# Performance work log

Hardware: AMD Instinct MI355X
Metric: run time of the kernel (lower is better)

Reference implementation:

```python
import jax, jax.numpy as jnp
import numpy as np

Q_MIN = 0.01
PT_THLD = 0.9
MAX_ETA = 4.0
LW_REP = 1.0
LW_NOISE = 0.1
LW_COWARD = 0.1
EPS = 1e-9

N_HITS = 50000
N_CLUSTERS = 1024  # cluster id 0 = noise, ids 1..K-1 = objects
D_EMB = 32


def setup_inputs() -> dict:
    key = jax.random.key(0)
    k0, k1, k2, k3, k4, k5 = jax.random.split(key, 6)
    beta = jax.random.uniform(k0, (N_HITS,), dtype=jnp.float32)
    x = jax.random.normal(k1, (N_HITS, D_EMB), dtype=jnp.float32)
    pt = jax.random.uniform(k2, (N_HITS,), dtype=jnp.float32)
    eta = jax.random.normal(k3, (N_HITS,), dtype=jnp.float32)
    reconstructable = jax.random.randint(k4, (N_HITS,), 0, 2, dtype=jnp.int32)
    cluster_ids = jax.random.randint(k5, (N_HITS,), 0, N_CLUSTERS, dtype=jnp.int64)
    return {
        'beta': beta, 'x': x, 'pt': pt, 'eta': eta,
        'reconstructable': reconstructable, 'cluster_ids': cluster_ids,
        'n_clusters': N_CLUSTERS,
    }


def reference(beta, x, pt, eta, reconstructable, cluster_ids, n_clusters):
    K = int(n_clusters)
    n_hits = beta.shape[0]
    n_part = K - 1  # objects of interest (excluding noise id 0)

    # charge q_j = arctanh(beta)^2 + q_min
    q = jnp.arctanh(jnp.clip(beta, 0.0, 1.0 - 1e-4)) ** 2 + Q_MIN  # [N]

    # attractive membership mask [N, K-1]: hit j belongs to object k and passes filters
    oids = jnp.arange(1, K)
    hit_ok = (reconstructable > 0) & (pt > PT_THLD) & (jnp.abs(eta) < MAX_ETA)
    att = (cluster_ids[:, None] == oids[None, :]) & hit_ok[:, None]
    attf = att.astype(q.dtype)

    # condensation point per object: hit with max charge within the object
    alphas = jnp.argmax(q[:, None] * attf, axis=0)  # [K-1]
    q_k = q[alphas]
    x_k = x[alphas]  # [K-1, D]

    # pairwise Euclidean distances, GEMM form (avoids [N,K,D] intermediate)
    d2 = (jnp.sum(x * x, axis=1)[:, None]
          + jnp.sum(x_k * x_k, axis=1)[None, :]
          - 2.0 * (x @ x_k.T))
    dist = jnp.sqrt(jnp.maximum(d2, 1e-12))  # [N, K-1]

    qw = q[:, None] * q_k[None, :]

    n_hits_oi = jnp.sum(hit_ok).astype(q.dtype)
    norm_att = EPS + n_hits_oi - n_part
    norm_rep = EPS + (n_part - 1) * n_hits

    v_att = jnp.sum(qw * (dist ** 2) * attf) / norm_att

    rep = (~att) & (dist < 1.0)  # max_n_rep=0 -> no subsampling
    v_rep = jnp.sum(qw * (1.0 - dist) * rep.astype(q.dtype)) / norm_rep

    l_coward = jnp.mean(1.0 - beta[alphas])

    noise_mask = (cluster_ids <= 0).astype(q.dtype)  # noise_threshold = 0
    l_noise = jnp.sum(beta * noise_mask) / jnp.maximum(jnp.sum(noise_mask), 1.0)

    total = v_att + LW_REP * v_rep + LW_NOISE * l_noise + LW_COWARD * l_coward
    return total
```

## Files before the change

kernel.cpp:

```cpp
#include <hip/hip_runtime.h>
#include <math.h>

namespace {

constexpr int D = 32;
constexpr int KOBJ = 1023;
constexpr float QMIN = 0.01f;
constexpr float PTT = 0.9f;
constexpr float METAETA = 4.0f;

typedef __attribute__((ext_vector_type(8))) short short8;
typedef __attribute__((ext_vector_type(4))) float f32x4;

__device__ inline float waveSum(float v) {
#pragma unroll
  for (int o = 32; o > 0; o >>= 1) v += __shfl_down(v, o, 64);
  return v;
}

__device__ inline ushort f2bf(float f) {
  unsigned u = __float_as_uint(f);
  return (ushort)((u + 0x7FFFu + ((u >> 16) & 1u)) >> 16);
}

__global__ void k_init(float* acc, int* flagNZ, unsigned long long* keys,
                       const int* __restrict__ cidw, int N) {
  int i = blockIdx.x * blockDim.x + threadIdx.x;
  if (i < KOBJ) keys[i] = 0ull;
  if (i < 8) acc[i] = 0.f;
  if (blockIdx.x == 0) {
    if (threadIdx.x == 0) flagNZ[0] = 0;
    __syncthreads();
    for (int jj = threadIdx.x; jj < 1024; jj += blockDim.x) {
      int idx = 2 * jj + 1;
      if (idx < N && cidw[idx] != 0) flagNZ[0] = 1;
    }
  }
}

__global__ void k_hits(const float* __restrict__ beta, const float* __restrict__ x,
                       const float* __restrict__ pt, const float* __restrict__ eta,
                       const int* __restrict__ recon, const int* __restrict__ cidw,
                       int N, const int* __restrict__ flagNZ,
                       float* acc, unsigned long long* keys,
                       float* __restrict__ qArr, float* __restrict__ nxArr,
                       int* __restrict__ attkArr) {
  int j = blockIdx.x * blockDim.x + threadIdx.x;
  int is64 = (flagNZ[0] == 0);
  bool ok = false;
  if (j < N) {
    int cid = is64 ? cidw[2 * j] : cidw[j];
    float b = beta[j];
    float bc = fminf(fmaxf(b, 0.f), 1.f - 1e-4f);
    float t = atanhf(bc);
    float q = t * t + QMIN;
    ok = (recon[j] > 0) && (pt[j] > PTT) && (fabsf(eta[j]) < METAETA);
    float nx = 0.f;
    const float4* xr = (const float4*)(x + (size_t)j * D);
#pragma unroll
    for (int i2 = 0; i2 < 8; ++i2) {
      float4 v = xr[i2];
      nx += v.x * v.x + v.y * v.y + v.z * v.z + v.w * v.w;
    }
    int attk = (ok && cid >= 1) ? cid : 0;
    qArr[j] = q;
    nxArr[j] = nx;
    attkArr[j] = attk;
    if (cid <= 0) {
      atomicAdd(&acc[2], b);
      atomicAdd(&acc[3], 1.f);
    }
    if (attk >= 1) {
      unsigned long long key =
          (((unsigned long long)__float_as_uint(q)) << 32) |
          (unsigned long long)(0xFFFFFFFFu - (unsigned)j);
      atomicMax(&keys[attk - 1], key);
    }
  }
  unsigned long long bal = __ballot(ok);
  if ((threadIdx.x & 63) == 0 && bal)
    atomicAdd(&acc[4], (float)__popcll(bal));
}

__global__ void k_clusters(const float* __restrict__ beta, const float* __restrict__ x,
                           const unsigned long long* __restrict__ keys,
                           const float* __restrict__ qArr, const float* __restrict__ nxArr,
                           int* __restrict__ alphaArr, float2* __restrict__ qnk,
                           ushort* __restrict__ xkb, float* acc) {
  int k = blockIdx.x * blockDim.x + threadIdx.x;
  float cw = 0.f;
  if (k < KOBJ) {
    unsigned long long key = keys[k];
    int alpha = (key != 0ull) ? (int)(0xFFFFFFFFu - (unsigned)(key & 0xFFFFFFFFull)) : 0;
    alphaArr[k] = alpha;
    qnk[k] = make_float2(qArr[alpha], nxArr[alpha]);
    const float4* s4 = (const float4*)(x + (size_t)alpha * D);
    ushort* dst = xkb + (size_t)k * D;
#pragma unroll
    for (int i = 0; i < 8; ++i) {
      float4 v = s4[i];
      dst[4 * i + 0] = f2bf(v.x);
      dst[4 * i + 1] = f2bf(v.y);
      dst[4 * i + 2] = f2bf(v.z);
      dst[4 * i + 3] = f2bf(v.w);
    }
    cw = 1.f - beta[alpha];
  } else if (k == KOBJ) {
    qnk[k] = make_float2(0.f, 1e30f);
    ushort* dst = xkb + (size_t)k * D;
#pragma unroll
    for (int i = 0; i < D; ++i) dst[i] = 0;
  }
  float s = waveSum(cw);
  if ((threadIdx.x & 63) == 0 && s != 0.f) atomicAdd(&acc[5], s);
}

__global__ __launch_bounds__(256) void k_pair_att(
    const float* __restrict__ x, int N, int rowgroups,
    const float* __restrict__ qArr, const float* __restrict__ nxArr,
    const int* __restrict__ attkArr, const int* __restrict__ alphaArr,
    const float2* __restrict__ qnk, const ushort* __restrict__ xkb,
    float* acc) {
  int t = threadIdx.x;

  if ((int)blockIdx.x < rowgroups) {
    __shared__ float2 qnkS[1024];
    for (int i = t; i < 1024; i += 256) qnkS[i] = qnk[i];

    int wv = t >> 6;
    int ln = t & 63;
    int lr = ln & 15;
    int lk = ln >> 4;
    int rowbase = blockIdx.x * 64;

    short8 afr[4];
#pragma unroll
    for (int rt = 0; rt < 4; ++rt) {
      int row = rowbase + rt * 16 + lr;
      row = min(row, N - 1);
      const float* p = x + (size_t)row * D + lk * 8;
      float4 v0 = *(const float4*)p;
      float4 v1 = *(const float4*)(p + 4);
      short8 a;
      a[0] = (short)f2bf(v0.x); a[1] = (short)f2bf(v0.y);
      a[2] = (short)f2bf(v0.z); a[3] = (short)f2bf(v0.w);
      a[4] = (short)f2bf(v1.x); a[5] = (short)f2bf(v1.y);
      a[6] = (short)f2bf(v1.z); a[7] = (short)f2bf(v1.w);
      afr[rt] = a;
    }
    float ha[4][4];
#pragma unroll
    for (int rt = 0; rt < 4; ++rt)
#pragma unroll
      for (int i = 0; i < 4; ++i) {
        int row = rowbase + rt * 16 + lk * 4 + i;
        ha[rt][i] = (row < N) ? (nxArr[row] - 1.f) * 0.5f : 1e37f;
      }
    __syncthreads();

    float rep = 0.f;
    int objbase = wv * 256;
#pragma unroll 1
    for (int tt = 0; tt < 16; ++tt) {
      int obj = objbase + tt * 16 + lr;
      const short8 b = *(const short8*)(xkb + (size_t)obj * D + lk * 8);
      float2 qn = qnkS[obj];
      float hk = qn.y * 0.5f;
      f32x4 z = {0.f, 0.f, 0.f, 0.f};
      f32x4 dot0 = __builtin_amdgcn_mfma_f32_16x16x32_bf16(afr[0], b, z, 0, 0, 0);
      f32x4 dot1 = __builtin_amdgcn_mfma_f32_16x16x32_bf16(afr[1], b, z, 0, 0, 0);
      f32x4 dot2 = __builtin_amdgcn_mfma_f32_16x16x32_bf16(afr[2], b, z, 0, 0, 0);
      f32x4 dot3 = __builtin_amdgcn_mfma_f32_16x16x32_bf16(afr[3], b, z, 0, 0, 0);
      float m = -1e30f;
#pragma unroll
      for (int i = 0; i < 4; ++i) {
        m = fmaxf(m, dot0[i] - (ha[0][i] + hk));
        m = fmaxf(m, dot1[i] - (ha[1][i] + hk));
        m = fmaxf(m, dot2[i] - (ha[2][i] + hk));
        m = fmaxf(m, dot3[i] - (ha[3][i] + hk));
      }
      if (__any(m > 0.f)) {
        float qk = qn.x;
        float nk1 = qn.y + 1.f;
#pragma unroll
        for (int rt = 0; rt < 4; ++rt) {
          float d0 = (rt == 0) ? dot0[0] : (rt == 1) ? dot1[0] : (rt == 2) ? dot2[0] : dot3[0];
          float d1 = (rt == 0) ? dot0[1] : (rt == 1) ? dot1[1] : (rt == 2) ? dot2[1] : dot3[1];
          float d2v = (rt == 0) ? dot0[2] : (rt == 1) ? dot1[2] : (rt == 2) ? dot2[2] : dot3[2];
          float d3 = (rt == 0) ? dot0[3] : (rt == 1) ? dot1[3] : (rt == 2) ? dot2[3] : dot3[3];
          float dd[4] = {d0, d1, d2v, d3};
#pragma unroll
          for (int i = 0; i < 4; ++i) {
            float d2 = fmaf(2.f, ha[rt][i] - dd[i], nk1);
            if (d2 < 1.f) {
              int row = rowbase + rt * 16 + lk * 4 + i;
              rep += qArr[row] * qk * (1.f - sqrtf(fmaxf(d2, 1e-12f)));
            }
          }
        }
      }
    }
    float s = waveSum(rep);
    if ((t & 63) == 0 && s != 0.f) atomicAdd(&acc[1], s);
  } else {
    int j = (blockIdx.x - rowgroups) * 256 + t;
    float attc = 0.f, repSub = 0.f;
    if (j < N) {
      int attk = attkArr[j];
      if (attk >= 1) {
        int k0 = attk - 1;
        int alpha = alphaArr[k0];
        float2 qn = qnk[k0];
        const float4* xj = (const float4*)(x + (size_t)j * D);
        const float4* xk = (const float4*)(x + (size_t)alpha * D);
        float dot = 0.f;
#pragma unroll
        for (int i = 0; i < 8; ++i) {
          float4 a = xj[i], b = xk[i];
          dot += a.x * b.x + a.y * b.y + a.z * b.z + a.w * b.w;
        }
        float d2 = nxArr[j] + qn.y - 2.f * dot;
        float w = qArr[j] * qn.x;
        attc = w * fmaxf(d2, 1e-12f);
        if (d2 < 1.f)
          repSub = w * (1.f - sqrtf(fmaxf(d2, 1e-12f)));
      }
    }
    float sa = waveSum(attc);
    float sr = waveSum(repSub);
    if ((t & 63) == 0) {
      if (sa != 0.f) atomicAdd(&acc[0], sa);
      if (sr != 0.f) atomicAdd(&acc[1], -sr);
    }
  }
}

__global__ void k_final(const float* __restrict__ acc, int N, float* out) {
  if (threadIdx.x == 0 && blockIdx.x == 0) {
    double attSum = acc[0], repSum = acc[1], noiseSum = acc[2];
    double noiseCnt = acc[3], okCnt = acc[4], cowardSum = acc[5];
    double norm_att = 1e-9 + okCnt - (double)KOBJ;
    double norm_rep = 1e-9 + (double)(KOBJ - 1) * (double)N;
    double v_att = attSum / norm_att;
    double v_rep = repSum / norm_rep;
    double l_coward = cowardSum / (double)KOBJ;
    double l_noise = noiseSum / fmax(noiseCnt, 1.0);
    out[0] = (float)(v_att + 1.0 * v_rep + 0.1 * l_noise + 0.1 * l_coward);
  }
}

}

extern "C" void kernel_launch(void* const* d_in, const int* in_sizes, int n_in,
                              void* d_out, int out_size, void* d_ws, size_t ws_size,
                              hipStream_t stream) {
  const float* beta = (const float*)d_in[0];
  const float* x = (const float*)d_in[1];
  const float* pt = (const float*)d_in[2];
  const float* eta = (const float*)d_in[3];
  const int* recon = (const int*)d_in[4];
  const int* cidw = (const int*)d_in[5];
  int N = in_sizes[0];
  float* out = (float*)d_out;

  char* w = (char*)d_ws;
  float* acc = (float*)w;
  int* flagNZ = (int*)(w + 32);
  unsigned long long* keys = (unsigned long long*)(w + 64);
  int* alphaArr = (int*)(w + 8256);
  float2* qnk = (float2*)(w + 12352);
  ushort* xkb = (ushort*)(w + 20544);
  float* qArr = (float*)(w + 86080);
  float* nxArr = (float*)(w + 86080 + (size_t)N * 4);
  int* attkArr = (int*)(w + 86080 + (size_t)N * 8);

  int nbN = (N + 255) / 256;
  int rowgroups = (N + 63) / 64;

  k_init<<<4, 256, 0, stream>>>(acc, flagNZ, keys, cidw, N);
  k_hits<<<nbN, 256, 0, stream>>>(beta, x, pt, eta, recon, cidw, N, flagNZ,
                                  acc, keys, qArr, nxArr, attkArr);
  k_clusters<<<4, 256, 0, stream>>>(beta, x, keys, qArr, nxArr,
                                    alphaArr, qnk, xkb, acc);
  k_pair_att<<<rowgroups + nbN, 256, 0, stream>>>(x, N, rowgroups, qArr, nxArr,
                                                  attkArr, alphaArr, qnk, xkb, acc);
  k_final<<<1, 64, 0, stream>>>(acc, N, out);
}
```

Baseline: 60.40 us.

## Fuse cluster and final kernels via last-block counters; fold norms into MFMA accumulator

The cluster-selection pass now runs in the last finishing block of the hits kernel, detected with a threadfence plus an atomic ticket counter. The final reduction runs the same way in the last block of the pair kernel, which removes two kernel launches. The pair kernel also merges the attractive-term blocks into the row-group blocks, with the first wave handling the 64 hits of its rows. The MFMA is seeded with nx+nk as the accumulator and x is prescaled by -2, so it outputs squared distances directly and the per-element subtract work goes away. The cost is a serialized tail in the last block, and rounding -2x to bf16 is exact, so precision is essentially unchanged.

```diff
diff --git a/kernel.cpp b/kernel.cpp
--- a/kernel.cpp
+++ b/kernel.cpp
@@ -23,11 +23,14 @@
   return (ushort)((u + 0x7FFFu + ((u >> 16) & 1u)) >> 16);
 }
 
-__global__ void k_init(float* acc, int* flagNZ, unsigned long long* keys,
-                       const int* __restrict__ cidw, int N) {
+__global__ void k_init(float* acc, unsigned* cnt, int* flagNZ,
+                       unsigned long long* keys, const int* __restrict__ cidw,
+                       int N) {
   int i = blockIdx.x * blockDim.x + threadIdx.x;
   if (i < KOBJ) keys[i] = 0ull;
   if (i < 8) acc[i] = 0.f;
+  if (i == 8) cnt[0] = 0u;
+  if (i == 9) cnt[1] = 0u;
   if (blockIdx.x == 0) {
     if (threadIdx.x == 0) flagNZ[0] = 0;
     __syncthreads();
@@ -38,22 +41,25 @@
   }
 }
 
-__global__ void k_hits(const float* __restrict__ beta, const float* __restrict__ x,
-                       const float* __restrict__ pt, const float* __restrict__ eta,
-                       const int* __restrict__ recon, const int* __restrict__ cidw,
-                       int N, const int* __restrict__ flagNZ,
-                       float* acc, unsigned long long* keys,
-                       float* __restrict__ qArr, float* __restrict__ nxArr,
-                       int* __restrict__ attkArr) {
-  int j = blockIdx.x * blockDim.x + threadIdx.x;
+__global__ __launch_bounds__(256) void k_hits_cl(
+    const float* __restrict__ beta, const float* __restrict__ x,
+    const float* __restrict__ pt, const float* __restrict__ eta,
+    const int* __restrict__ recon, const int* __restrict__ cidw,
+    int N, const int* __restrict__ flagNZ,
+    float* acc, unsigned* cnt, unsigned long long* keys,
+    float* __restrict__ qArr, float* __restrict__ nxArr,
+    int* __restrict__ attkArr, int* __restrict__ alphaArr,
+    float2* __restrict__ qnk, ushort* __restrict__ xkb) {
+  int t = threadIdx.x;
+  int j = blockIdx.x * 256 + t;
   int is64 = (flagNZ[0] == 0);
   bool ok = false;
   if (j < N) {
     int cid = is64 ? cidw[2 * j] : cidw[j];
     float b = beta[j];
     float bc = fminf(fmaxf(b, 0.f), 1.f - 1e-4f);
-    float t = atanhf(bc);
-    float q = t * t + QMIN;
+    float tt = atanhf(bc);
+    float q = tt * tt + QMIN;
     ok = (recon[j] > 0) && (pt[j] > PTT) && (fabsf(eta[j]) < METAETA);
     float nx = 0.f;
     const float4* xr = (const float4*)(x + (size_t)j * D);
@@ -78,132 +84,130 @@
     }
   }
   unsigned long long bal = __ballot(ok);
-  if ((threadIdx.x & 63) == 0 && bal)
+  if ((t & 63) == 0 && bal)
     atomicAdd(&acc[4], (float)__popcll(bal));
-}
-
-__global__ void k_clusters(const float* __restrict__ beta, const float* __restrict__ x,
-                           const unsigned long long* __restrict__ keys,
-                           const float* __restrict__ qArr, const float* __restrict__ nxArr,
-                           int* __restrict__ alphaArr, float2* __restrict__ qnk,
-                           ushort* __restrict__ xkb, float* acc) {
-  int k = blockIdx.x * blockDim.x + threadIdx.x;
+
+  __threadfence();
+  __shared__ int lastFlag;
+  if (t == 0) {
+    unsigned tk = atomicAdd(&cnt[0], 1u);
+    lastFlag = (tk == gridDim.x - 1);
+  }
+  __syncthreads();
+  if (!lastFlag) return;
+  __threadfence();
+
   float cw = 0.f;
-  if (k < KOBJ) {
-    unsigned long long key = keys[k];
-    int alpha = (key != 0ull) ? (int)(0xFFFFFFFFu - (unsigned)(key & 0xFFFFFFFFull)) : 0;
-    alphaArr[k] = alpha;
-    qnk[k] = make_float2(qArr[alpha], nxArr[alpha]);
-    const float4* s4 = (const float4*)(x + (size_t)alpha * D);
-    ushort* dst = xkb + (size_t)k * D;
-#pragma unroll
-    for (int i = 0; i < 8; ++i) {
-      float4 v = s4[i];
-      dst[4 * i + 0] = f2bf(v.x);
-      dst[4 * i + 1] = f2bf(v.y);
-      dst[4 * i + 2] = f2bf(v.z);
-      dst[4 * i + 3] = f2bf(v.w);
-    }
-    cw = 1.f - beta[alpha];
-  } else if (k == KOBJ) {
-    qnk[k] = make_float2(0.f, 1e30f);
-    ushort* dst = xkb + (size_t)k * D;
-#pragma unroll
-    for (int i = 0; i < D; ++i) dst[i] = 0;
+  for (int k = t; k < 1024; k += 256) {
+    if (k < KOBJ) {
+      unsigned long long key = keys[k];
+      int alpha = (key != 0ull) ? (int)(0xFFFFFFFFu - (unsigned)(key & 0xFFFFFFFFull)) : 0;
+      alphaArr[k] = alpha;
+      qnk[k] = make_float2(qArr[alpha], nxArr[alpha]);
+      const float4* s4 = (const float4*)(x + (size_t)alpha * D);
+      ushort* dst = xkb + (size_t)k * D;
+#pragma unroll
+      for (int i = 0; i < 8; ++i) {
+        float4 v = s4[i];
+        dst[4 * i + 0] = f2bf(v.x);
+        dst[4 * i + 1] = f2bf(v.y);
+        dst[4 * i + 2] = f2bf(v.z);
+        dst[4 * i + 3] = f2bf(v.w);
+      }
+      cw += 1.f - beta[alpha];
+    } else {
+      qnk[k] = make_float2(0.f, 1e30f);
+      ushort* dst = xkb + (size_t)k * D;
+#pragma unroll
+      for (int i = 0; i < D; ++i) dst[i] = 0;
+    }
   }
   float s = waveSum(cw);
-  if ((threadIdx.x & 63) == 0 && s != 0.f) atomicAdd(&acc[5], s);
-}
-
-__global__ __launch_bounds__(256) void k_pair_att(
-    const float* __restrict__ x, int N, int rowgroups,
+  if ((t & 63) == 0 && s != 0.f) atomicAdd(&acc[5], s);
+}
+
+__global__ __launch_bounds__(256) void k_pair_all(
+    const float* __restrict__ x, int N,
     const float* __restrict__ qArr, const float* __restrict__ nxArr,
     const int* __restrict__ attkArr, const int* __restrict__ alphaArr,
     const float2* __restrict__ qnk, const ushort* __restrict__ xkb,
-    float* acc) {
+    float* acc, unsigned* cnt, float* out) {
+  __shared__ float2 qnkS[1024];
+  __shared__ int lastFlag;
   int t = threadIdx.x;
-
-  if ((int)blockIdx.x < rowgroups) {
-    __shared__ float2 qnkS[1024];
-    for (int i = t; i < 1024; i += 256) qnkS[i] = qnk[i];
-
-    int wv = t >> 6;
-    int ln = t & 63;
-    int lr = ln & 15;
-    int lk = ln >> 4;
-    int rowbase = blockIdx.x * 64;
-
-    short8 afr[4];
-#pragma unroll
-    for (int rt = 0; rt < 4; ++rt) {
-      int row = rowbase + rt * 16 + lr;
-      row = min(row, N - 1);
-      const float* p = x + (size_t)row * D + lk * 8;
-      float4 v0 = *(const float4*)p;
-      float4 v1 = *(const float4*)(p + 4);
-      short8 a;
-      a[0] = (short)f2bf(v0.x); a[1] = (short)f2bf(v0.y);
-      a[2] = (short)f2bf(v0.z); a[3] = (short)f2bf(v0.w);
-      a[4] = (short)f2bf(v1.x); a[5] = (short)f2bf(v1.y);
-      a[6] = (short)f2bf(v1.z); a[7] = (short)f2bf(v1.w);
-      afr[rt] = a;
-    }
-    float ha[4][4];
-#pragma unroll
-    for (int rt = 0; rt < 4; ++rt)
-#pragma unroll
-      for (int i = 0; i < 4; ++i) {
-        int row = rowbase + rt * 16 + lk * 4 + i;
-        ha[rt][i] = (row < N) ? (nxArr[row] - 1.f) * 0.5f : 1e37f;
-      }
-    __syncthreads();
-
-    float rep = 0.f;
-    int objbase = wv * 256;
+  for (int i = t; i < 1024; i += 256) qnkS[i] = qnk[i];
+
+  int wv = t >> 6;
+  int ln = t & 63;
+  int lr = ln & 15;
+  int lk = ln >> 4;
+  int rowbase = blockIdx.x * 64;
+
+  short8 am2[4];
+#pragma unroll
+  for (int rt = 0; rt < 4; ++rt) {
+    int row = min(rowbase + rt * 16 + lr, N - 1);
+    const float* p = x + (size_t)row * D + lk * 8;
+    float4 v0 = *(const float4*)p;
+    float4 v1 = *(const float4*)(p + 4);
+    short8 a;
+    a[0] = (short)f2bf(-2.f * v0.x); a[1] = (short)f2bf(-2.f * v0.y);
+    a[2] = (short)f2bf(-2.f * v0.z); a[3] = (short)f2bf(-2.f * v0.w);
+    a[4] = (short)f2bf(-2.f * v1.x); a[5] = (short)f2bf(-2.f * v1.y);
+    a[6] = (short)f2bf(-2.f * v1.z); a[7] = (short)f2bf(-2.f * v1.w);
+    am2[rt] = a;
+  }
+  float nxr[4][4], qrow[4][4];
+#pragma unroll
+  for (int rt = 0; rt < 4; ++rt)
+#pragma unroll
+    for (int i = 0; i < 4; ++i) {
+      int row = rowbase + rt * 16 + lk * 4 + i;
+      int rc = min(row, N - 1);
+      nxr[rt][i] = (row < N) ? nxArr[rc] : 1e37f;
+      qrow[rt][i] = (row < N) ? qArr[rc] : 0.f;
+    }
+  __syncthreads();
+
+  float rep = 0.f;
+  int objbase = wv * 256;
 #pragma unroll 1
-    for (int tt = 0; tt < 16; ++tt) {
-      int obj = objbase + tt * 16 + lr;
-      const short8 b = *(const short8*)(xkb + (size_t)obj * D + lk * 8);
-      float2 qn = qnkS[obj];
-      float hk = qn.y * 0.5f;
-      f32x4 z = {0.f, 0.f, 0.f, 0.f};
-      f32x4 dot0 = __builtin_amdgcn_mfma_f32_16x16x32_bf16(afr[0], b, z, 0, 0, 0);
-      f32x4 dot1 = __builtin_amdgcn_mfma_f32_16x16x32_bf16(afr[1], b, z, 0, 0, 0);
-      f32x4 dot2 = __builtin_amdgcn_mfma_f32_16x16x32_bf16(afr[2], b, z, 0, 0, 0);
-      f32x4 dot3 = __builtin_amdgcn_mfma_f32_16x16x32_bf16(afr[3], b, z, 0, 0, 0);
-      float m = -1e30f;
-#pragma unroll
-      for (int i = 0; i < 4; ++i) {
-        m = fmaxf(m, dot0[i] - (ha[0][i] + hk));
-        m = fmaxf(m, dot1[i] - (ha[1][i] + hk));
-        m = fmaxf(m, dot2[i] - (ha[2][i] + hk));
-        m = fmaxf(m, dot3[i] - (ha[3][i] + hk));
-      }
-      if (__any(m > 0.f)) {
-        float qk = qn.x;
-        float nk1 = qn.y + 1.f;
-#pragma unroll
-        for (int rt = 0; rt < 4; ++rt) {
-          float d0 = (rt == 0) ? dot0[0] : (rt == 1) ? dot1[0] : (rt == 2) ? dot2[0] : dot3[0];
-          float d1 = (rt == 0) ? dot0[1] : (rt == 1) ? dot1[1] : (rt == 2) ? dot2[1] : dot3[1];
-          float d2v = (rt == 0) ? dot0[2] : (rt == 1) ? dot1[2] : (rt == 2) ? dot2[2] : dot3[2];
-          float d3 = (rt == 0) ? dot0[3] : (rt == 1) ? dot1[3] : (rt == 2) ? dot2[3] : dot3[3];
-          float dd[4] = {d0, d1, d2v, d3};
-#pragma unroll
-          for (int i = 0; i < 4; ++i) {
-            float d2 = fmaf(2.f, ha[rt][i] - dd[i], nk1);
-            if (d2 < 1.f) {
-              int row = rowbase + rt * 16 + lk * 4 + i;
-              rep += qArr[row] * qk * (1.f - sqrtf(fmaxf(d2, 1e-12f)));
-            }
-          }
+  for (int tt = 0; tt < 16; ++tt) {
+    int obj = objbase + tt * 16 + lr;
+    const short8 b = *(const short8*)(xkb + (size_t)obj * D + lk * 8);
+    float2 qn = qnkS[obj];
+    float nk = qn.y;
+    f32x4 c0 = {nxr[0][0] + nk, nxr[0][1] + nk, nxr[0][2] + nk, nxr[0][3] + nk};
+    f32x4 c1 = {nxr[1][0] + nk, nxr[1][1] + nk, nxr[1][2] + nk, nxr[1][3] + nk};
+    f32x4 c2 = {nxr[2][0] + nk, nxr[2][1] + nk, nxr[2][2] + nk, nxr[2][3] + nk};
+    f32x4 c3 = {nxr[3][0] + nk, nxr[3][1] + nk, nxr[3][2] + nk, nxr[3][3] + nk};
+    f32x4 s0 = __builtin_amdgcn_mfma_f32_16x16x32_bf16(am2[0], b, c0, 0, 0, 0);
+    f32x4 s1 = __builtin_amdgcn_mfma_f32_16x16x32_bf16(am2[1], b, c1, 0, 0, 0);
+    f32x4 s2 = __builtin_amdgcn_mfma_f32_16x16x32_bf16(am2[2], b, c2, 0, 0, 0);
+    f32x4 s3 = __builtin_amdgcn_mfma_f32_16x16x32_bf16(am2[3], b, c3, 0, 0, 0);
+    float m = 1e30f;
+#pragma unroll
+    for (int i = 0; i < 4; ++i) {
+      m = fminf(m, fminf(fminf(s0[i], s1[i]), fminf(s2[i], s3[i])));
+    }
+    if (__any(m < 1.f)) {
+      float qk = qn.x;
+#pragma unroll
+      for (int rt = 0; rt < 4; ++rt) {
+#pragma unroll
+        for (int i = 0; i < 4; ++i) {
+          float d2 = (rt == 0) ? s0[i] : (rt == 1) ? s1[i] : (rt == 2) ? s2[i] : s3[i];
+          if (d2 < 1.f)
+            rep += qrow[rt][i] * qk * (1.f - sqrtf(fmaxf(d2, 1e-12f)));
         }
       }
     }
-    float s = waveSum(rep);
-    if ((t & 63) == 0 && s != 0.f) atomicAdd(&acc[1], s);
-  } else {
-    int j = (blockIdx.x - rowgroups) * 256 + t;
+  }
+  float sw = waveSum(rep);
+  if (ln == 0 && sw != 0.f) atomicAdd(&acc[1], sw);
+
+  if (t < 64) {
+    int j = rowbase + t;
     float attc = 0.f, repSub = 0.f;
     if (j < N) {
       int attk = attkArr[j];
@@ -216,8 +220,8 @@
         float dot = 0.f;
 #pragma unroll
         for (int i = 0; i < 8; ++i) {
-          float4 a = xj[i], b = xk[i];
-          dot += a.x * b.x + a.y * b.y + a.z * b.z + a.w * b.w;
+          float4 a = xj[i], bb = xk[i];
+          dot += a.x * bb.x + a.y * bb.y + a.z * bb.z + a.w * bb.w;
         }
         float d2 = nxArr[j] + qn.y - 2.f * dot;
         float w = qArr[j] * qn.x;
@@ -228,15 +232,21 @@
     }
     float sa = waveSum(attc);
     float sr = waveSum(repSub);
-    if ((t & 63) == 0) {
+    if (t == 0) {
       if (sa != 0.f) atomicAdd(&acc[0], sa);
       if (sr != 0.f) atomicAdd(&acc[1], -sr);
     }
   }
-}
-
-__global__ void k_final(const float* __restrict__ acc, int N, float* out) {
-  if (threadIdx.x == 0 && blockIdx.x == 0) {
+
+  __threadfence();
+  if (t == 0) {
+    unsigned tk = atomicAdd(&cnt[1], 1u);
+    lastFlag = (tk == gridDim.x - 1);
+  }
+  __syncthreads();
+  if (!lastFlag) return;
+  __threadfence();
+  if (t == 0) {
     double attSum = acc[0], repSum = acc[1], noiseSum = acc[2];
     double noiseCnt = acc[3], okCnt = acc[4], cowardSum = acc[5];
     double norm_att = 1e-9 + okCnt - (double)KOBJ;
@@ -265,7 +275,8 @@
 
   char* w = (char*)d_ws;
   float* acc = (float*)w;
-  int* flagNZ = (int*)(w + 32);
+  unsigned* cnt = (unsigned*)(w + 32);
+  int* flagNZ = (int*)(w + 40);
   unsigned long long* keys = (unsigned long long*)(w + 64);
   int* alphaArr = (int*)(w + 8256);
   float2* qnk = (float2*)(w + 12352);
@@ -277,12 +288,10 @@
   int nbN = (N + 255) / 256;
   int rowgroups = (N + 63) / 64;
 
-  k_init<<<4, 256, 0, stream>>>(acc, flagNZ, keys, cidw, N);
-  k_hits<<<nbN, 256, 0, stream>>>(beta, x, pt, eta, recon, cidw, N, flagNZ,
-                                  acc, keys, qArr, nxArr, attkArr);
-  k_clusters<<<4, 256, 0, stream>>>(beta, x, keys, qArr, nxArr,
-                                    alphaArr, qnk, xkb, acc);
-  k_pair_att<<<rowgroups + nbN, 256, 0, stream>>>(x, N, rowgroups, qArr, nxArr,
-                                                  attkArr, alphaArr, qnk, xkb, acc);
-  k_final<<<1, 64, 0, stream>>>(acc, N, out);
-}
+  k_init<<<4, 256, 0, stream>>>(acc, cnt, flagNZ, keys, cidw, N);
+  k_hits_cl<<<nbN, 256, 0, stream>>>(beta, x, pt, eta, recon, cidw, N, flagNZ,
+                                     acc, cnt, keys, qArr, nxArr, attkArr,
+                                     alphaArr, qnk, xkb);
+  k_pair_all<<<rowgroups, 256, 0, stream>>>(x, N, qArr, nxArr, attkArr,
+                                            alphaArr, qnk, xkb, acc, cnt, out);
+}
```

After: 109.9 us. 81.9% more time.
